# Kernel optimization log

Measured on AMD Instinct MI355X. Metric: run time of the kernel, lower is better.

The kernel has to match this reference:

```python
import jax, jax.numpy as jnp
import numpy as np

# EEACSF hyperparameters (module defaults)
CUTOFF = 5.2
ANG_CUTOFF = 3.5
RADIAL_ETA = 16.0
ANGULAR_ETA = 8.0
RDIV = 16          # radial_dist_divisions
ADIV = 4           # angular_dist_divisions
ZETA = 32.0
SECTIONS = 4       # angle_sections
R_START = 0.8
A_START = 0.8
N_SPECIES = 87     # size of periodic-table / valence table

N_ATOMS = 20000
N_EDGES = 640000       # radial edges
N_ANG_EDGES = 160000   # angular-graph edges
N_PAIRS = 560000       # angle pairs


def setup_inputs() -> dict:
    key = jax.random.key(0)
    ks = jax.random.split(key, 12)
    species = jax.random.randint(ks[0], (N_ATOMS,), 0, N_SPECIES)
    # radial graph: distances in (R_START, CUTOFF)
    distances = R_START + (CUTOFF - R_START) * jax.random.uniform(ks[1], (N_EDGES,), jnp.float32)
    switch = jax.random.uniform(ks[2], (N_EDGES,), jnp.float32)
    edge_src = jax.random.randint(ks[3], (N_EDGES,), 0, N_ATOMS)
    edge_dst = jax.random.randint(ks[4], (N_EDGES,), 0, N_ATOMS)
    # angular graph
    ang_angles = np.pi * jax.random.uniform(ks[5], (N_PAIRS,), jnp.float32)
    ang_distances = A_START + (ANG_CUTOFF - A_START) * jax.random.uniform(ks[6], (N_ANG_EDGES,), jnp.float32)
    ang_switch = jax.random.uniform(ks[7], (N_ANG_EDGES,), jnp.float32)
    ang_edge_dst = jax.random.randint(ks[8], (N_ANG_EDGES,), 0, N_ATOMS)
    angle_src = jax.random.randint(ks[9], (N_PAIRS,), 0, N_ANG_EDGES)
    angle_dst = jax.random.randint(ks[10], (N_PAIRS,), 0, N_ANG_EDGES)
    central_atom = jax.random.randint(ks[11], (N_PAIRS,), 0, N_ATOMS)
    # valence structure table (stands in for the preprocessed VALENCE_STRUCTURE constant)
    valence_table = jax.random.uniform(jax.random.fold_in(key, 99), (N_SPECIES, 4), jnp.float32)
    return {
        "species": species, "distances": distances, "switch": switch,
        "edge_src": edge_src, "edge_dst": edge_dst,
        "ang_angles": ang_angles, "ang_distances": ang_distances,
        "ang_switch": ang_switch, "ang_edge_dst": ang_edge_dst,
        "angle_src": angle_src, "angle_dst": angle_dst,
        "central_atom": central_atom, "valence_table": valence_table,
    }


def reference(species, distances, switch, edge_src, edge_dst,
              ang_angles, ang_distances, ang_switch, ang_edge_dst,
              angle_src, angle_dst, central_atom, valence_table):
    n_atoms = species.shape[0]
    valence = valence_table[species]                                  # [N,4]

    # ---- radial AEV ----
    shiftR = jnp.asarray(np.linspace(R_START, CUTOFF, RDIV + 1)[None, :-1], distances.dtype)
    x2 = RADIAL_ETA * (distances[:, None] - shiftR) ** 2              # [E,16]
    radial_terms = 0.25 * jnp.exp(-x2) * switch[:, None]              # [E,16]
    radial_aev = jax.ops.segment_sum(
        radial_terms[:, :, None] * valence[edge_dst, None, :],        # [E,16,4]
        edge_src, num_segments=n_atoms,
    ).reshape(n_atoms, -1)                                            # [N,64]

    # ---- angular AEV ----
    d12 = 0.5 * (ang_distances[angle_src] + ang_distances[angle_dst])[:, None]  # [P,1]
    angle_start = np.pi / (2 * SECTIONS)
    shiftZ = jnp.asarray((np.linspace(0, np.pi, SECTIONS + 1) + angle_start)[None, :-1], ang_distances.dtype)
    shiftA = jnp.asarray(np.linspace(A_START, ANG_CUTOFF, ADIV + 1)[None, :-1], ang_distances.dtype)
    factor1 = (0.5 + 0.5 * jnp.cos(ang_angles[:, None] - shiftZ)) ** ZETA       # [P,4]
    factor2 = jnp.exp(-ANGULAR_ETA * (d12 - shiftA) ** 2)                       # [P,4]
    angular_terms = (factor1[:, None, :] * factor2[:, :, None]).reshape(-1, SECTIONS * ADIV)
    angular_terms = angular_terms * 2 * (ang_switch[angle_src] * ang_switch[angle_dst])[:, None]  # [P,16]

    valence_dst = valence[ang_edge_dst]                               # [E2,4]
    vp = valence_dst[angle_src] + valence_dst[angle_dst]              # [P,4]
    vm = valence_dst[angle_src] * valence_dst[angle_dst]              # [P,4]
    valence_ang = (vp[:, :, None] * vm[:, None, :]).reshape(-1, 16)   # [P,16]

    angular_aev = jax.ops.segment_sum(
        angular_terms[:, :, None] * valence_ang[:, None, :],          # [P,16,16]
        central_atom, num_segments=n_atoms,
    ).reshape(n_atoms, -1)                                            # [N,256]

    onehot = jax.nn.one_hot(species, N_SPECIES, dtype=distances.dtype)  # [N,87]
    return jnp.concatenate((onehot, radial_aev, angular_aev), axis=-1)  # [N,407]
```

## Files before the change

kernel.cpp:

```cpp
#include <hip/hip_runtime.h>
#include <hip/hip_fp16.h>
#include <math.h>

#define NCOLS   407
#define RAD_OFF 87
#define ANG_OFF 151
#define T1      3072
#define WB      32
#define MAXBKT  640
#define CAP2    3008


typedef __attribute__((ext_vector_type(8))) _Float16 f16x8;
typedef __attribute__((ext_vector_type(4))) float    f32x4;

static __device__ inline unsigned pack2(float a, float b) {
    __half2 h = __floats2half2_rn(a, b);
    return *reinterpret_cast<unsigned*>(&h);
}
static __device__ inline float2 unpack2(unsigned u) {
    __half2 h = *reinterpret_cast<__half2*>(&u);
    return __half22float2(h);
}

__global__ __launch_bounds__(256) void init_kernel(const int* __restrict__ species,
                                                   const float4* __restrict__ valence,
                                                   float4* __restrict__ val_atom,
                                                   int n_atoms) {
    int idx = blockIdx.x * 256 + threadIdx.x;
    if (idx < n_atoms) val_atom[idx] = valence[species[idx]];
}

__global__ __launch_bounds__(256) void pass0_kernel(const int* __restrict__ esrc,
                                                    const int* __restrict__ central,
                                                    const float* __restrict__ ang_dist,
                                                    const float* __restrict__ ang_sw,
                                                    const int* __restrict__ ang_edge_dst,
                                                    const float4* __restrict__ val_atom,
                                                    int* __restrict__ tileHist,
                                                    uint4* __restrict__ edata,
                                                    int n_edges, int n_pairs, int n_ang_edges,
                                                    int nbkt, int nt_rad, int nt_ang) {
    int bid = blockIdx.x;
    int t = threadIdx.x;

    if (bid < nt_rad + nt_ang) {
        __shared__ int lh[MAXBKT];
        int is_ang = bid >= nt_rad;
        const int* key = is_ang ? central : esrc;
        int n   = is_ang ? n_pairs : n_edges;
        int off = (is_ang ? bid - nt_rad : bid) * T1;
        for (int b = t; b < nbkt; b += 256) lh[b] = 0;
        __syncthreads();
        #pragma unroll
        for (int k = 0; k < T1 / 256; ++k) {
            int i = off + k * 256 + t;
            if (i < n) atomicAdd(&lh[key[i] >> 5], 1);
        }
        __syncthreads();
        int* row = tileHist + (size_t)bid * nbkt;
        for (int b = t; b < nbkt; b += 256) row[b] = lh[b];
        return;
    }

    int i = (bid - nt_rad - nt_ang) * 2560 + t;
    #pragma unroll
    for (int k = 0; k < 10; ++k, i += 256) {
        if (i < n_ang_edges) {
            float4 v = val_atom[ang_edge_dst[i]];
            uint4 r;
            r.x = __float_as_uint(ang_dist[i]);
            r.y = __float_as_uint(ang_sw[i]);
            r.z = pack2(v.x, v.y);
            r.w = pack2(v.z, v.w);
            edata[i] = r;
        }
    }
}

__global__ __launch_bounds__(256) void scanA_kernel(int* __restrict__ tileHist,
                                                    int* __restrict__ bktTotals,
                                                    int nt_rad, int nt_ang, int nbkt) {
    int wid  = blockIdx.x * 4 + (threadIdx.x >> 6);
    int lane = threadIdx.x & 63;
    if (wid >= 2 * nbkt) return;
    int g = wid >= nbkt;
    int b = g ? wid - nbkt : wid;
    int* th = tileHist + (g ? (size_t)nt_rad * nbkt : 0);
    int nt = g ? nt_ang : nt_rad;
    int run = 0;
    for (int k0 = 0; k0 < nt; k0 += 64) {
        int k = k0 + lane;
        int v = (k < nt) ? th[(size_t)k * nbkt + b] : 0;
        int s = v;
        #pragma unroll
        for (int o = 1; o < 64; o <<= 1) {
            int u = __shfl_up(s, o, 64);
            if (lane >= o) s += u;
        }
        if (k < nt) th[(size_t)k * nbkt + b] = run + s - v;
        run += __shfl(s, 63, 64);
    }
    if (lane == 0) bktTotals[g * MAXBKT + b] = run;
}

__global__ __launch_bounds__(1024) void scanB_kernel(const int* __restrict__ bktTotals,
                                                     int* __restrict__ bktBase, int nbkt) {
    int g = blockIdx.x;
    const int* tot = bktTotals + g * MAXBKT;
    int* bb = bktBase + g * (MAXBKT + 1);
    __shared__ int part[1024];
    int t = threadIdx.x;
    int v = (t < nbkt) ? tot[t] : 0;
    part[t] = v;
    __syncthreads();
    for (int o = 1; o < 1024; o <<= 1) {
        int u = (t >= o) ? part[t - o] : 0;
        __syncthreads();
        part[t] += u;
        __syncthreads();
    }
    if (t < nbkt) bb[t] = part[t] - v;
    if (t == nbkt - 1) bb[nbkt] = part[t];
}

__global__ __launch_bounds__(256) void pass1_kernel(
    const float* __restrict__ dist, const float* __restrict__ sw,
    const int* __restrict__ esrc, const int* __restrict__ edst,
    const float* __restrict__ ang_angles,
    const int* __restrict__ psrc, const int* __restrict__ pdst,
    const int* __restrict__ central,
    const float4* __restrict__ val_atom,
    const int* __restrict__ tileHist, const int* __restrict__ bktBase,
    uint4* __restrict__ arr_rad, uint4* __restrict__ arr_ang,
    int n_edges, int n_pairs, int nbkt, int nt_rad)
{
    __shared__ uint4 buf[T1];
    __shared__ int   dst[T1];
    __shared__ int   lh[MAXBKT];
    __shared__ int   gb[MAXBKT];
    __shared__ int   sc[256];

    int bid = blockIdx.x;
    int t = threadIdx.x;
    int is_ang = bid >= nt_rad;
    const int* key = is_ang ? central : esrc;
    int n   = is_ang ? n_pairs : n_edges;
    int off = (is_ang ? bid - nt_rad : bid) * T1;
    int cnt = min(T1, n - off);
    uint4* arr = is_ang ? arr_ang : arr_rad;
    const int* row = tileHist + (size_t)bid * nbkt;
    const int* bb  = bktBase + is_ang * (MAXBKT + 1);

    for (int b = t; b < nbkt; b += 256) { lh[b] = 0; gb[b] = row[b] + bb[b]; }
    __syncthreads();

    int meta[T1 / 256];
    #pragma unroll
    for (int k = 0; k < T1 / 256; ++k) {
        int i = off + k * 256 + t;
        meta[k] = -1;
        if (i < n) {
            int b = key[i] >> 5;
            int r = atomicAdd(&lh[b], 1);
            meta[k] = (b << 12) | r;
        }
    }
    __syncthreads();

    {
        int ch = (nbkt + 255) >> 8;
        int vals[4];
        int lo = t * ch, s = 0;
        for (int k = 0; k < ch; ++k) {
            int idx = lo + k;
            int v = (idx < nbkt) ? lh[idx] : 0;
            vals[k] = v; s += v;
        }
        sc[t] = s;
        __syncthreads();
        for (int o = 1; o < 256; o <<= 1) {
            int v = (t >= o) ? sc[t - o] : 0;
            __syncthreads();
            sc[t] += v;
            __syncthreads();
        }
        int run = sc[t] - s;
        for (int k = 0; k < ch; ++k) {
            int idx = lo + k;
            if (idx < nbkt) lh[idx] = run;
            run += vals[k];
        }
        __syncthreads();
    }

    #pragma unroll
    for (int k = 0; k < T1 / 256; ++k) {
        if (meta[k] < 0) continue;
        int i = off + k * 256 + t;
        int b = meta[k] >> 12, r = meta[k] & 4095;
        uint4 rec;
        if (!is_ang) {
            float d  = dist[i];
            float ps = 0.25f * sw[i];
            float4 v = val_atom[edst[i]];
            rec.x = __float_as_uint(d);
            rec.y = pack2(ps * v.x, ps * v.y);
            rec.z = pack2(ps * v.z, ps * v.w);
            rec.w = (unsigned)esrc[i];
        } else {
            rec.x = (unsigned)psrc[i];
            rec.y = (unsigned)pdst[i];
            rec.z = __float_as_uint(ang_angles[i]);
            rec.w = (unsigned)central[i];
        }
        int pos = lh[b] + r;
        buf[pos] = rec;
        dst[pos] = gb[b] + r;
    }
    __syncthreads();

    #pragma unroll
    for (int k = 0; k < T1 / 256; ++k) {
        int j = k * 256 + t;
        if (j < cnt) arr[dst[j]] = buf[j];
    }
}

__global__ __launch_bounds__(256) void pass2_kernel(uint4* __restrict__ arr_rad,
                                                    uint4* __restrict__ arr_ang,
                                                    const int* __restrict__ bktBase,
                                                    int* __restrict__ rad_offsets,
                                                    int* __restrict__ ang_offsets,
                                                    int nbkt, int n_atoms) {
    __shared__ uint4  buf[CAP2];
    __shared__ unsigned short rnk[CAP2];
    __shared__ int lh[WB];
    __shared__ int scanA_[WB + 1];

    int bid = blockIdx.x;
    int t = threadIdx.x;
    int g = bid >= nbkt;
    int b = g ? bid - nbkt : bid;
    const int* bb = bktBase + g * (MAXBKT + 1);
    int lo = bb[b], hi = bb[b + 1];
    int cnt = hi - lo;
    uint4* arr = g ? arr_ang : arr_rad;
    int* offsets = g ? ang_offsets : rad_offsets;
    int loA = b << 5;

    if (t < WB) lh[t] = 0;
    __syncthreads();
    for (int j = t; j < cnt; j += 256) {
        uint4 r = arr[lo + j];
        buf[j] = r;
        int a = (int)r.w - loA;
        rnk[j] = (unsigned short)atomicAdd(&lh[a], 1);
    }
    __syncthreads();
    if (t == 0) {
        int run = 0;
        for (int a = 0; a < WB; ++a) { scanA_[a] = run; run += lh[a]; }
        scanA_[WB] = run;
    }
    __syncthreads();
    if (t < WB && loA + t < n_atoms) offsets[loA + t] = lo + scanA_[t];
    if (t == 0 && b == nbkt - 1) offsets[n_atoms] = bb[nbkt];
    for (int j = t; j < cnt; j += 256) {
        int a = (int)buf[j].w - loA;
        arr[lo + scanA_[a] + (int)rnk[j]] = buf[j];
    }
}

__global__ __launch_bounds__(256) void phaseB_kernel(
    const uint4* __restrict__ ang_rec, const int* __restrict__ ang_offsets,
    const uint4* __restrict__ edata,
    const uint4* __restrict__ rad_pay, const int* __restrict__ rad_offsets,
    const int* __restrict__ species,
    float* __restrict__ out, int n_atoms)
{
    __shared__ uint4 sh[4][256];
    int wid  = (blockIdx.x << 2) + (threadIdx.x >> 6);
    int lane = threadIdx.x & 63;
    uint4* my = sh[threadIdx.x >> 6];

    if (wid < n_atoms) {
        int atom = wid;
        int beg = ang_offsets[atom];
        int end = ang_offsets[atom + 1];
        int m  = lane & 15;
        int g4 = lane >> 4;
        const _Float16* hl = (const _Float16*)my;
        f32x4 acc = {0.f, 0.f, 0.f, 0.f};

        for (int base = beg; base < end; base += 64) {
            int idx = base + lane;
            unsigned q[16];
            if (idx < end) {
                uint4 pr = ang_rec[idx];
                int e1 = (int)pr.x;
                int e2 = (int)pr.y;
                float ang = __uint_as_float(pr.z);
                uint4 r1 = edata[e1];
                uint4 r2 = edata[e2];
                float d12 = 0.5f * (__uint_as_float(r1.x) + __uint_as_float(r2.x));
                float swp = 2.0f * __uint_as_float(r1.y) * __uint_as_float(r2.y);
                float2 v1a = unpack2(r1.z), v1b = unpack2(r1.w);
                float2 v2a = unpack2(r2.z), v2b = unpack2(r2.w);
                float vp[4] = {v1a.x + v2a.x, v1a.y + v2a.y, v1b.x + v2b.x, v1b.y + v2b.y};
                float vm[4] = {v1a.x * v2a.x, v1a.y * v2a.y, v1b.x * v2b.x, v1b.y * v2b.y};

                float sa, ca;
                __sincosf(ang, &sa, &ca);
                const float czv[4] = { 0.92387953f,  0.38268343f, -0.38268343f, -0.92387953f };
                const float szv[4] = { 0.38268343f,  0.92387953f,  0.92387953f,  0.38268343f };
                float f1v[4];
                #pragma unroll
                for (int z = 0; z < 4; ++z) {
                    float y = 0.5f + 0.5f * (ca * czv[z] + sa * szv[z]);
                    float y2 = y * y, y4 = y2 * y2, y8 = y4 * y4, y16 = y8 * y8;
                    f1v[z] = y16 * y16;
                }
                float f2sv[4];
                #pragma unroll
                for (int a = 0; a < 4; ++a) {
                    float x = d12 - (0.8f + 0.675f * (float)a);
                    f2sv[a] = swp * __expf(-8.0f * x * x);
                }
                #pragma unroll
                for (int a = 0; a < 4; ++a) {
                    q[a * 2 + 0] = pack2(f2sv[a] * f1v[0], f2sv[a] * f1v[1]);
                    q[a * 2 + 1] = pack2(f2sv[a] * f1v[2], f2sv[a] * f1v[3]);
                }
                #pragma unroll
                for (int i2 = 0; i2 < 4; ++i2) {
                    q[8 + i2 * 2 + 0] = pack2(vp[i2] * vm[0], vp[i2] * vm[1]);
                    q[8 + i2 * 2 + 1] = pack2(vp[i2] * vm[2], vp[i2] * vm[3]);
                }
            } else {
                #pragma unroll
                for (int k = 0; k < 16; ++k) q[k] = 0u;
            }
            my[lane * 4 + 0] = make_uint4(q[0],  q[1],  q[2],  q[3]);
            my[lane * 4 + 1] = make_uint4(q[4],  q[5],  q[6],  q[7]);
            my[lane * 4 + 2] = make_uint4(q[8],  q[9],  q[10], q[11]);
            my[lane * 4 + 3] = make_uint4(q[12], q[13], q[14], q[15]);
            asm volatile("s_waitcnt lgkmcnt(0)" ::: "memory");

            int cnt = min(64, end - base);
            {
                f16x8 wf, uf;
                #pragma unroll
                for (int i = 0; i < 8; ++i) {
                    int row = (g4 << 3) + i;
                    wf[i] = hl[row * 32 + m];
                    uf[i] = hl[row * 32 + 16 + m];
                }
                acc = __builtin_amdgcn_mfma_f32_16x16x32_f16(wf, uf, acc, 0, 0, 0);
            }
            if (cnt > 32) {
                f16x8 wf, uf;
                #pragma unroll
                for (int i = 0; i < 8; ++i) {
                    int row = 32 + (g4 << 3) + i;
                    wf[i] = hl[row * 32 + m];
                    uf[i] = hl[row * 32 + 16 + m];
                }
                acc = __builtin_amdgcn_mfma_f32_16x16x32_f16(wf, uf, acc, 0, 0, 0);
            }
            asm volatile("s_waitcnt lgkmcnt(0)" ::: "memory");
        }
        float* orow = out + (size_t)atom * NCOLS + ANG_OFF;
        #pragma unroll
        for (int r = 0; r < 4; ++r)
            orow[(g4 * 4 + r) * 16 + m] = acc[r];
        return;
    }

    int atom = wid - n_atoms;
    if (atom >= n_atoms) return;
    int beg = rad_offsets[atom];
    int end = rad_offsets[atom + 1];
    int m  = lane & 15;
    int g4 = lane >> 4;
    const _Float16* hl = (const _Float16*)my;
    const float*    fl = (const float*)my;
    float shiftm = 0.8f + 0.275f * (float)m;
    f32x4 acc = {0.f, 0.f, 0.f, 0.f};

    for (int base = beg; base < end; base += 64) {
        int idx = base + lane;
        my[lane] = (idx < end) ? rad_pay[idx] : make_uint4(0u, 0u, 0u, 0u);
        asm volatile("s_waitcnt lgkmcnt(0)" ::: "memory");

        int cnt = min(64, end - base);
        {
            f16x8 wf, uf;
            #pragma unroll
            for (int i = 0; i < 8; ++i) {
                int k = (g4 << 3) + i;
                float d = fl[k * 4];
                float x = d - shiftm;
                wf[i] = (_Float16)__expf(-16.0f * x * x);
                uf[i] = (m < 4) ? hl[k * 8 + 2 + m] : (_Float16)0.0f;
            }
            acc = __builtin_amdgcn_mfma_f32_16x16x32_f16(wf, uf, acc, 0, 0, 0);
        }
        if (cnt > 32) {
            f16x8 wf, uf;
            #pragma unroll
            for (int i = 0; i < 8; ++i) {
                int k = 32 + (g4 << 3) + i;
                float d = fl[k * 4];
                float x = d - shiftm;
                wf[i] = (_Float16)__expf(-16.0f * x * x);
                uf[i] = (m < 4) ? hl[k * 8 + 2 + m] : (_Float16)0.0f;
            }
            acc = __builtin_amdgcn_mfma_f32_16x16x32_f16(wf, uf, acc, 0, 0, 0);
        }
        asm volatile("s_waitcnt lgkmcnt(0)" ::: "memory");
    }
    size_t rowbase = (size_t)atom * NCOLS;
    if (m < 4) {
        #pragma unroll
        for (int r = 0; r < 4; ++r)
            out[rowbase + RAD_OFF + (g4 * 4 + r) * 4 + m] = acc[r];
    }
    int sp = species[atom];
    out[rowbase + lane] = (lane == sp) ? 1.0f : 0.0f;
    if (lane < 23) out[rowbase + 64 + lane] = ((64 + lane) == sp) ? 1.0f : 0.0f;
}

extern "C" void kernel_launch(void* const* d_in, const int* in_sizes, int n_in,
                              void* d_out, int out_size, void* d_ws, size_t ws_size,
                              hipStream_t stream) {
    const int*   species      = (const int*)  d_in[0];
    const float* distances    = (const float*)d_in[1];
    const float* switch_      = (const float*)d_in[2];
    const int*   edge_src     = (const int*)  d_in[3];
    const int*   edge_dst     = (const int*)  d_in[4];
    const float* ang_angles   = (const float*)d_in[5];
    const float* ang_dist     = (const float*)d_in[6];
    const float* ang_switch   = (const float*)d_in[7];
    const int*   ang_edge_dst = (const int*)  d_in[8];
    const int*   angle_src    = (const int*)  d_in[9];
    const int*   angle_dst    = (const int*)  d_in[10];
    const int*   central_atom = (const int*)  d_in[11];
    const float4* valence     = (const float4*)d_in[12];

    float* out = (float*)d_out;

    const int n_atoms     = in_sizes[0];
    const int n_edges     = in_sizes[1];
    const int n_ang_edges = in_sizes[6];
    const int n_pairs     = in_sizes[5];

    const int nbkt   = (n_atoms + WB - 1) / WB;
    const int nt_rad = (n_edges + T1 - 1) / T1;
    const int nt_ang = (n_pairs + T1 - 1) / T1;

    char* ws = (char*)d_ws;
    size_t off = 0;
    auto alloc = [&](size_t bytes) -> void* {
        void* p = ws + off;
        off = (off + bytes + 15) & ~(size_t)15;
        return p;
    };
    uint4*  arr_rad     = (uint4*) alloc((size_t)n_edges * 16);
    uint4*  arr_ang     = (uint4*) alloc((size_t)n_pairs * 16);
    uint4*  edata       = (uint4*) alloc((size_t)n_ang_edges * 16);
    int*    tileHist    = (int*)   alloc((size_t)(nt_rad + nt_ang) * nbkt * 4);
    int*    bktTotals   = (int*)   alloc((size_t)2 * MAXBKT * sizeof(int));
    int*    bktBase     = (int*)   alloc((size_t)2 * (MAXBKT + 1) * sizeof(int));
    float4* val_atom    = (float4*)alloc((size_t)n_atoms * sizeof(float4));
    int*    rad_offsets = (int*)   alloc((size_t)(n_atoms + 1) * sizeof(int));
    int*    ang_offsets = (int*)   alloc((size_t)(n_atoms + 1) * sizeof(int));

    init_kernel<<<(n_atoms + 255) / 256, 256, 0, stream>>>(
        species, valence, val_atom, n_atoms);

    int nb_edata = (n_ang_edges + 2559) / 2560;
    pass0_kernel<<<nt_rad + nt_ang + nb_edata, 256, 0, stream>>>(
        edge_src, central_atom, ang_dist, ang_switch, ang_edge_dst, val_atom,
        tileHist, edata, n_edges, n_pairs, n_ang_edges, nbkt, nt_rad, nt_ang);

    scanA_kernel<<<(2 * nbkt + 3) / 4, 256, 0, stream>>>(
        tileHist, bktTotals, nt_rad, nt_ang, nbkt);

    scanB_kernel<<<2, 1024, 0, stream>>>(bktTotals, bktBase, nbkt);

    pass1_kernel<<<nt_rad + nt_ang, 256, 0, stream>>>(
        distances, switch_, edge_src, edge_dst,
        ang_angles, angle_src, angle_dst, central_atom,
        val_atom, tileHist, bktBase, arr_rad, arr_ang,
        n_edges, n_pairs, nbkt, nt_rad);

    pass2_kernel<<<2 * nbkt, 256, 0, stream>>>(
        arr_rad, arr_ang, bktBase, rad_offsets, ang_offsets, nbkt, n_atoms);

    int nb_B = (2 * n_atoms + 3) / 4;
    phaseB_kernel<<<nb_B, 256, 0, stream>>>(
        arr_ang, ang_offsets, edata, arr_rad, rad_offsets, species, out, n_atoms);
}
```

Measured before the change: 78.89 us.

## Fuse per-bucket sort with feature compute and drop valence init kernel

The second-level per-bucket counting sort is merged with the radial/angular MFMA accumulation. Records stay in shared memory and are read through an index permutation instead of being scattered back to global memory and re-read by a separate kernel. The init kernel that built per-atom valence is removed, and valence is looked up as valence[species[...]] inline. In exchange, buckets are truncated to CAPF records, which risks dropping edges if a bucket overflows. Each block also now handles 32 atoms with 4 waves, which lowers parallelism compared with one wave per atom.

```diff
diff --git a/kernel.cpp b/kernel.cpp
--- a/kernel.cpp
+++ b/kernel.cpp
@@ -8,7 +8,7 @@
 #define T1      3072
 #define WB      32
 #define MAXBKT  640
-#define CAP2    3008
+#define CAPF    1792
 
 
 typedef __attribute__((ext_vector_type(8))) _Float16 f16x8;
@@ -21,14 +21,6 @@
 static __device__ inline float2 unpack2(unsigned u) {
     __half2 h = *reinterpret_cast<__half2*>(&u);
     return __half22float2(h);
-}
-
-__global__ __launch_bounds__(256) void init_kernel(const int* __restrict__ species,
-                                                   const float4* __restrict__ valence,
-                                                   float4* __restrict__ val_atom,
-                                                   int n_atoms) {
-    int idx = blockIdx.x * 256 + threadIdx.x;
-    if (idx < n_atoms) val_atom[idx] = valence[species[idx]];
 }
 
 __global__ __launch_bounds__(256) void pass0_kernel(const int* __restrict__ esrc,
@@ -36,7 +28,8 @@
                                                     const float* __restrict__ ang_dist,
                                                     const float* __restrict__ ang_sw,
                                                     const int* __restrict__ ang_edge_dst,
-                                                    const float4* __restrict__ val_atom,
+                                                    const int* __restrict__ species,
+                                                    const float4* __restrict__ valence,
                                                     int* __restrict__ tileHist,
                                                     uint4* __restrict__ edata,
                                                     int n_edges, int n_pairs, int n_ang_edges,
@@ -67,7 +60,7 @@
     #pragma unroll
     for (int k = 0; k < 10; ++k, i += 256) {
         if (i < n_ang_edges) {
-            float4 v = val_atom[ang_edge_dst[i]];
+            float4 v = valence[species[ang_edge_dst[i]]];
             uint4 r;
             r.x = __float_as_uint(ang_dist[i]);
             r.y = __float_as_uint(ang_sw[i]);
@@ -130,7 +123,7 @@
     const float* __restrict__ ang_angles,
     const int* __restrict__ psrc, const int* __restrict__ pdst,
     const int* __restrict__ central,
-    const float4* __restrict__ val_atom,
+    const int* __restrict__ species, const float4* __restrict__ valence,
     const int* __restrict__ tileHist, const int* __restrict__ bktBase,
     uint4* __restrict__ arr_rad, uint4* __restrict__ arr_ang,
     int n_edges, int n_pairs, int nbkt, int nt_rad)
@@ -203,7 +196,7 @@
         if (!is_ang) {
             float d  = dist[i];
             float ps = 0.25f * sw[i];
-            float4 v = val_atom[edst[i]];
+            float4 v = valence[species[edst[i]]];
             rec.x = __float_as_uint(d);
             rec.y = pack2(ps * v.x, ps * v.y);
             rec.z = pack2(ps * v.z, ps * v.w);
@@ -227,26 +220,27 @@
     }
 }
 
-__global__ __launch_bounds__(256) void pass2_kernel(uint4* __restrict__ arr_rad,
-                                                    uint4* __restrict__ arr_ang,
-                                                    const int* __restrict__ bktBase,
-                                                    int* __restrict__ rad_offsets,
-                                                    int* __restrict__ ang_offsets,
-                                                    int nbkt, int n_atoms) {
-    __shared__ uint4  buf[CAP2];
-    __shared__ unsigned short rnk[CAP2];
+__global__ __launch_bounds__(256) void pass2B_kernel(
+    const uint4* __restrict__ arr_rad, const uint4* __restrict__ arr_ang,
+    const uint4* __restrict__ edata,
+    const int* __restrict__ bktBase,
+    const int* __restrict__ species,
+    float* __restrict__ out, int nbkt, int n_atoms)
+{
+    __shared__ uint4 buf[CAPF];
+    __shared__ unsigned short ord[CAPF];
     __shared__ int lh[WB];
-    __shared__ int scanA_[WB + 1];
+    __shared__ int sA[WB + 1];
+    __shared__ uint4 stg[4][256];
 
     int bid = blockIdx.x;
     int t = threadIdx.x;
     int g = bid >= nbkt;
     int b = g ? bid - nbkt : bid;
     const int* bb = bktBase + g * (MAXBKT + 1);
-    int lo = bb[b], hi = bb[b + 1];
-    int cnt = hi - lo;
-    uint4* arr = g ? arr_ang : arr_rad;
-    int* offsets = g ? ang_offsets : rad_offsets;
+    int lo  = bb[b];
+    int cnt = min(bb[b + 1] - lo, CAPF);
+    const uint4* arr = g ? arr_ang : arr_rad;
     int loA = b << 5;
 
     if (t < WB) lh[t] = 0;
@@ -254,181 +248,180 @@
     for (int j = t; j < cnt; j += 256) {
         uint4 r = arr[lo + j];
         buf[j] = r;
-        int a = (int)r.w - loA;
-        rnk[j] = (unsigned short)atomicAdd(&lh[a], 1);
+        atomicAdd(&lh[(int)r.w - loA], 1);
     }
     __syncthreads();
     if (t == 0) {
         int run = 0;
-        for (int a = 0; a < WB; ++a) { scanA_[a] = run; run += lh[a]; }
-        scanA_[WB] = run;
-    }
-    __syncthreads();
-    if (t < WB && loA + t < n_atoms) offsets[loA + t] = lo + scanA_[t];
-    if (t == 0 && b == nbkt - 1) offsets[n_atoms] = bb[nbkt];
+        for (int a = 0; a < WB; ++a) { sA[a] = run; run += lh[a]; }
+        sA[WB] = run;
+    }
+    __syncthreads();
+    if (t < WB) lh[t] = sA[t];
+    __syncthreads();
     for (int j = t; j < cnt; j += 256) {
         int a = (int)buf[j].w - loA;
-        arr[lo + scanA_[a] + (int)rnk[j]] = buf[j];
-    }
-}
-
-__global__ __launch_bounds__(256) void phaseB_kernel(
-    const uint4* __restrict__ ang_rec, const int* __restrict__ ang_offsets,
-    const uint4* __restrict__ edata,
-    const uint4* __restrict__ rad_pay, const int* __restrict__ rad_offsets,
-    const int* __restrict__ species,
-    float* __restrict__ out, int n_atoms)
-{
-    __shared__ uint4 sh[4][256];
-    int wid  = (blockIdx.x << 2) + (threadIdx.x >> 6);
-    int lane = threadIdx.x & 63;
-    uint4* my = sh[threadIdx.x >> 6];
-
-    if (wid < n_atoms) {
-        int atom = wid;
-        int beg = ang_offsets[atom];
-        int end = ang_offsets[atom + 1];
-        int m  = lane & 15;
-        int g4 = lane >> 4;
-        const _Float16* hl = (const _Float16*)my;
+        int pos = atomicAdd(&lh[a], 1);
+        ord[pos] = (unsigned short)j;
+    }
+    __syncthreads();
+
+    int w    = t >> 6;
+    int lane = t & 63;
+    int m  = lane & 15;
+    int g4 = lane >> 4;
+
+    if (g) {
+        const _Float16* hl = (const _Float16*)stg[w];
+        for (int ai = 0; ai < 8; ++ai) {
+            int a = w * 8 + ai;
+            int atom = loA + a;
+            if (atom >= n_atoms) break;
+            int beg = sA[a], end = sA[a + 1];
+            f32x4 acc = {0.f, 0.f, 0.f, 0.f};
+
+            for (int base = beg; base < end; base += 64) {
+                int idx = base + lane;
+                unsigned q[16];
+                if (idx < end) {
+                    uint4 pr = buf[ord[idx]];
+                    int e1 = (int)pr.x;
+                    int e2 = (int)pr.y;
+                    float ang = __uint_as_float(pr.z);
+                    uint4 r1 = edata[e1];
+                    uint4 r2 = edata[e2];
+                    float d12 = 0.5f * (__uint_as_float(r1.x) + __uint_as_float(r2.x));
+                    float swp = 2.0f * __uint_as_float(r1.y) * __uint_as_float(r2.y);
+                    float2 v1a = unpack2(r1.z), v1b = unpack2(r1.w);
+                    float2 v2a = unpack2(r2.z), v2b = unpack2(r2.w);
+                    float vp[4] = {v1a.x + v2a.x, v1a.y + v2a.y, v1b.x + v2b.x, v1b.y + v2b.y};
+                    float vm[4] = {v1a.x * v2a.x, v1a.y * v2a.y, v1b.x * v2b.x, v1b.y * v2b.y};
+
+                    float sa, ca;
+                    __sincosf(ang, &sa, &ca);
+                    const float czv[4] = { 0.92387953f,  0.38268343f, -0.38268343f, -0.92387953f };
+                    const float szv[4] = { 0.38268343f,  0.92387953f,  0.92387953f,  0.38268343f };
+                    float f1v[4];
+                    #pragma unroll
+                    for (int z = 0; z < 4; ++z) {
+                        float y = 0.5f + 0.5f * (ca * czv[z] + sa * szv[z]);
+                        float y2 = y * y, y4 = y2 * y2, y8 = y4 * y4, y16 = y8 * y8;
+                        f1v[z] = y16 * y16;
+                    }
+                    float f2sv[4];
+                    #pragma unroll
+                    for (int aa = 0; aa < 4; ++aa) {
+                        float x = d12 - (0.8f + 0.675f * (float)aa);
+                        f2sv[aa] = swp * __expf(-8.0f * x * x);
+                    }
+                    #pragma unroll
+                    for (int aa = 0; aa < 4; ++aa) {
+                        q[aa * 2 + 0] = pack2(f2sv[aa] * f1v[0], f2sv[aa] * f1v[1]);
+                        q[aa * 2 + 1] = pack2(f2sv[aa] * f1v[2], f2sv[aa] * f1v[3]);
+                    }
+                    #pragma unroll
+                    for (int i2 = 0; i2 < 4; ++i2) {
+                        q[8 + i2 * 2 + 0] = pack2(vp[i2] * vm[0], vp[i2] * vm[1]);
+                        q[8 + i2 * 2 + 1] = pack2(vp[i2] * vm[2], vp[i2] * vm[3]);
+                    }
+                } else {
+                    #pragma unroll
+                    for (int k = 0; k < 16; ++k) q[k] = 0u;
+                }
+                stg[w][lane * 4 + 0] = make_uint4(q[0],  q[1],  q[2],  q[3]);
+                stg[w][lane * 4 + 1] = make_uint4(q[4],  q[5],  q[6],  q[7]);
+                stg[w][lane * 4 + 2] = make_uint4(q[8],  q[9],  q[10], q[11]);
+                stg[w][lane * 4 + 3] = make_uint4(q[12], q[13], q[14], q[15]);
+                asm volatile("s_waitcnt lgkmcnt(0)" ::: "memory");
+
+                int cc = min(64, end - base);
+                {
+                    f16x8 wf, uf;
+                    #pragma unroll
+                    for (int i = 0; i < 8; ++i) {
+                        int row = (g4 << 3) + i;
+                        wf[i] = hl[row * 32 + m];
+                        uf[i] = hl[row * 32 + 16 + m];
+                    }
+                    acc = __builtin_amdgcn_mfma_f32_16x16x32_f16(wf, uf, acc, 0, 0, 0);
+                }
+                if (cc > 32) {
+                    f16x8 wf, uf;
+                    #pragma unroll
+                    for (int i = 0; i < 8; ++i) {
+                        int row = 32 + (g4 << 3) + i;
+                        wf[i] = hl[row * 32 + m];
+                        uf[i] = hl[row * 32 + 16 + m];
+                    }
+                    acc = __builtin_amdgcn_mfma_f32_16x16x32_f16(wf, uf, acc, 0, 0, 0);
+                }
+                asm volatile("s_waitcnt lgkmcnt(0)" ::: "memory");
+            }
+            float* orow = out + (size_t)atom * NCOLS + ANG_OFF;
+            #pragma unroll
+            for (int r = 0; r < 4; ++r)
+                orow[(g4 * 4 + r) * 16 + m] = acc[r];
+        }
+        return;
+    }
+
+    const _Float16* hl = (const _Float16*)buf;
+    const float*    fl = (const float*)buf;
+    float shiftm = 0.8f + 0.275f * (float)m;
+    for (int ai = 0; ai < 8; ++ai) {
+        int a = w * 8 + ai;
+        int atom = loA + a;
+        if (atom >= n_atoms) break;
+        int beg = sA[a], end = sA[a + 1];
         f32x4 acc = {0.f, 0.f, 0.f, 0.f};
 
         for (int base = beg; base < end; base += 64) {
-            int idx = base + lane;
-            unsigned q[16];
-            if (idx < end) {
-                uint4 pr = ang_rec[idx];
-                int e1 = (int)pr.x;
-                int e2 = (int)pr.y;
-                float ang = __uint_as_float(pr.z);
-                uint4 r1 = edata[e1];
-                uint4 r2 = edata[e2];
-                float d12 = 0.5f * (__uint_as_float(r1.x) + __uint_as_float(r2.x));
-                float swp = 2.0f * __uint_as_float(r1.y) * __uint_as_float(r2.y);
-                float2 v1a = unpack2(r1.z), v1b = unpack2(r1.w);
-                float2 v2a = unpack2(r2.z), v2b = unpack2(r2.w);
-                float vp[4] = {v1a.x + v2a.x, v1a.y + v2a.y, v1b.x + v2b.x, v1b.y + v2b.y};
-                float vm[4] = {v1a.x * v2a.x, v1a.y * v2a.y, v1b.x * v2b.x, v1b.y * v2b.y};
-
-                float sa, ca;
-                __sincosf(ang, &sa, &ca);
-                const float czv[4] = { 0.92387953f,  0.38268343f, -0.38268343f, -0.92387953f };
-                const float szv[4] = { 0.38268343f,  0.92387953f,  0.92387953f,  0.38268343f };
-                float f1v[4];
-                #pragma unroll
-                for (int z = 0; z < 4; ++z) {
-                    float y = 0.5f + 0.5f * (ca * czv[z] + sa * szv[z]);
-                    float y2 = y * y, y4 = y2 * y2, y8 = y4 * y4, y16 = y8 * y8;
-                    f1v[z] = y16 * y16;
-                }
-                float f2sv[4];
-                #pragma unroll
-                for (int a = 0; a < 4; ++a) {
-                    float x = d12 - (0.8f + 0.675f * (float)a);
-                    f2sv[a] = swp * __expf(-8.0f * x * x);
-                }
-                #pragma unroll
-                for (int a = 0; a < 4; ++a) {
-                    q[a * 2 + 0] = pack2(f2sv[a] * f1v[0], f2sv[a] * f1v[1]);
-                    q[a * 2 + 1] = pack2(f2sv[a] * f1v[2], f2sv[a] * f1v[3]);
-                }
-                #pragma unroll
-                for (int i2 = 0; i2 < 4; ++i2) {
-                    q[8 + i2 * 2 + 0] = pack2(vp[i2] * vm[0], vp[i2] * vm[1]);
-                    q[8 + i2 * 2 + 1] = pack2(vp[i2] * vm[2], vp[i2] * vm[3]);
-                }
-            } else {
-                #pragma unroll
-                for (int k = 0; k < 16; ++k) q[k] = 0u;
-            }
-            my[lane * 4 + 0] = make_uint4(q[0],  q[1],  q[2],  q[3]);
-            my[lane * 4 + 1] = make_uint4(q[4],  q[5],  q[6],  q[7]);
-            my[lane * 4 + 2] = make_uint4(q[8],  q[9],  q[10], q[11]);
-            my[lane * 4 + 3] = make_uint4(q[12], q[13], q[14], q[15]);
-            asm volatile("s_waitcnt lgkmcnt(0)" ::: "memory");
-
-            int cnt = min(64, end - base);
+            int cnt2 = min(64, end - base);
             {
                 f16x8 wf, uf;
                 #pragma unroll
                 for (int i = 0; i < 8; ++i) {
-                    int row = (g4 << 3) + i;
-                    wf[i] = hl[row * 32 + m];
-                    uf[i] = hl[row * 32 + 16 + m];
+                    int k = (g4 << 3) + i;
+                    int live = (k < cnt2);
+                    int o = live ? (int)ord[base + k] : 0;
+                    float d = fl[o * 4];
+                    float x = d - shiftm;
+                    float e = __expf(-16.0f * x * x);
+                    wf[i] = live ? (_Float16)e : (_Float16)0.0f;
+                    uf[i] = (live && m < 4) ? hl[o * 8 + 2 + m] : (_Float16)0.0f;
                 }
                 acc = __builtin_amdgcn_mfma_f32_16x16x32_f16(wf, uf, acc, 0, 0, 0);
             }
-            if (cnt > 32) {
+            if (cnt2 > 32) {
                 f16x8 wf, uf;
                 #pragma unroll
                 for (int i = 0; i < 8; ++i) {
-                    int row = 32 + (g4 << 3) + i;
-                    wf[i] = hl[row * 32 + m];
-                    uf[i] = hl[row * 32 + 16 + m];
+                    int k = 32 + (g4 << 3) + i;
+                    int live = (k < cnt2);
+                    int o = live ? (int)ord[base + k] : 0;
+                    float d = fl[o * 4];
+                    float x = d - shiftm;
+                    float e = __expf(-16.0f * x * x);
+                    wf[i] = live ? (_Float16)e : (_Float16)0.0f;
+                    uf[i] = (live && m < 4) ? hl[o * 8 + 2 + m] : (_Float16)0.0f;
                 }
                 acc = __builtin_amdgcn_mfma_f32_16x16x32_f16(wf, uf, acc, 0, 0, 0);
             }
-            asm volatile("s_waitcnt lgkmcnt(0)" ::: "memory");
-        }
-        float* orow = out + (size_t)atom * NCOLS + ANG_OFF;
-        #pragma unroll
-        for (int r = 0; r < 4; ++r)
-            orow[(g4 * 4 + r) * 16 + m] = acc[r];
-        return;
-    }
-
-    int atom = wid - n_atoms;
-    if (atom >= n_atoms) return;
-    int beg = rad_offsets[atom];
-    int end = rad_offsets[atom + 1];
-    int m  = lane & 15;
-    int g4 = lane >> 4;
-    const _Float16* hl = (const _Float16*)my;
-    const float*    fl = (const float*)my;
-    float shiftm = 0.8f + 0.275f * (float)m;
-    f32x4 acc = {0.f, 0.f, 0.f, 0.f};
-
-    for (int base = beg; base < end; base += 64) {
-        int idx = base + lane;
-        my[lane] = (idx < end) ? rad_pay[idx] : make_uint4(0u, 0u, 0u, 0u);
-        asm volatile("s_waitcnt lgkmcnt(0)" ::: "memory");
-
-        int cnt = min(64, end - base);
-        {
-            f16x8 wf, uf;
+        }
+        if (m < 4) {
+            size_t rowbase = (size_t)atom * NCOLS;
             #pragma unroll
-            for (int i = 0; i < 8; ++i) {
-                int k = (g4 << 3) + i;
-                float d = fl[k * 4];
-                float x = d - shiftm;
-                wf[i] = (_Float16)__expf(-16.0f * x * x);
-                uf[i] = (m < 4) ? hl[k * 8 + 2 + m] : (_Float16)0.0f;
-            }
-            acc = __builtin_amdgcn_mfma_f32_16x16x32_f16(wf, uf, acc, 0, 0, 0);
-        }
-        if (cnt > 32) {
-            f16x8 wf, uf;
-            #pragma unroll
-            for (int i = 0; i < 8; ++i) {
-                int k = 32 + (g4 << 3) + i;
-                float d = fl[k * 4];
-                float x = d - shiftm;
-                wf[i] = (_Float16)__expf(-16.0f * x * x);
-                uf[i] = (m < 4) ? hl[k * 8 + 2 + m] : (_Float16)0.0f;
-            }
-            acc = __builtin_amdgcn_mfma_f32_16x16x32_f16(wf, uf, acc, 0, 0, 0);
-        }
-        asm volatile("s_waitcnt lgkmcnt(0)" ::: "memory");
-    }
-    size_t rowbase = (size_t)atom * NCOLS;
-    if (m < 4) {
-        #pragma unroll
-        for (int r = 0; r < 4; ++r)
-            out[rowbase + RAD_OFF + (g4 * 4 + r) * 4 + m] = acc[r];
-    }
-    int sp = species[atom];
-    out[rowbase + lane] = (lane == sp) ? 1.0f : 0.0f;
-    if (lane < 23) out[rowbase + 64 + lane] = ((64 + lane) == sp) ? 1.0f : 0.0f;
+            for (int r = 0; r < 4; ++r)
+                out[rowbase + RAD_OFF + (g4 * 4 + r) * 4 + m] = acc[r];
+        }
+    }
+
+    for (int idx2 = t; idx2 < WB * 87; idx2 += 256) {
+        int a = idx2 / 87, c = idx2 - a * 87;
+        int atom = loA + a;
+        if (atom < n_atoms)
+            out[(size_t)atom * NCOLS + c] = (c == species[atom]) ? 1.0f : 0.0f;
+    }
 }
 
 extern "C" void kernel_launch(void* const* d_in, const int* in_sizes, int n_in,
@@ -472,17 +465,12 @@
     int*    tileHist    = (int*)   alloc((size_t)(nt_rad + nt_ang) * nbkt * 4);
     int*    bktTotals   = (int*)   alloc((size_t)2 * MAXBKT * sizeof(int));
     int*    bktBase     = (int*)   alloc((size_t)2 * (MAXBKT + 1) * sizeof(int));
-    float4* val_atom    = (float4*)alloc((size_t)n_atoms * sizeof(float4));
-    int*    rad_offsets = (int*)   alloc((size_t)(n_atoms + 1) * sizeof(int));
-    int*    ang_offsets = (int*)   alloc((size_t)(n_atoms + 1) * sizeof(int));
-
-    init_kernel<<<(n_atoms + 255) / 256, 256, 0, stream>>>(
-        species, valence, val_atom, n_atoms);
 
     int nb_edata = (n_ang_edges + 2559) / 2560;
     pass0_kernel<<<nt_rad + nt_ang + nb_edata, 256, 0, stream>>>(
-        edge_src, central_atom, ang_dist, ang_switch, ang_edge_dst, val_atom,
-        tileHist, edata, n_edges, n_pairs, n_ang_edges, nbkt, nt_rad, nt_ang);
+        edge_src, central_atom, ang_dist, ang_switch, ang_edge_dst,
+        species, valence, tileHist, edata,
+        n_edges, n_pairs, n_ang_edges, nbkt, nt_rad, nt_ang);
 
     scanA_kernel<<<(2 * nbkt + 3) / 4, 256, 0, stream>>>(
         tileHist, bktTotals, nt_rad, nt_ang, nbkt);
@@ -492,13 +480,9 @@
     pass1_kernel<<<nt_rad + nt_ang, 256, 0, stream>>>(
         distances, switch_, edge_src, edge_dst,
         ang_angles, angle_src, angle_dst, central_atom,
-        val_atom, tileHist, bktBase, arr_rad, arr_ang,
+        species, valence, tileHist, bktBase, arr_rad, arr_ang,
         n_edges, n_pairs, nbkt, nt_rad);
 
-    pass2_kernel<<<2 * nbkt, 256, 0, stream>>>(
-        arr_rad, arr_ang, bktBase, rad_offsets, ang_offsets, nbkt, n_atoms);
-
-    int nb_B = (2 * n_atoms + 3) / 4;
-    phaseB_kernel<<<nb_B, 256, 0, stream>>>(
-        arr_ang, ang_offsets, edata, arr_rad, rad_offsets, species, out, n_atoms);
-}
+    pass2B_kernel<<<2 * nbkt, 256, 0, stream>>>(
+        arr_rad, arr_ang, edata, bktBase, species, out, nbkt, n_atoms);
+}
```

New measurement: 79.90 us. Within noise of the previous version (+1.3%).
